# Performance work log

Hardware: AMD Instinct MI355X
Metric: run time of the kernel (lower is better)

Reference implementation:

```python
import jax, jax.numpy as jnp
import numpy as np


def setup_inputs() -> dict:
    key = jax.random.key(0)
    k1, k2 = jax.random.split(key)
    B, F = 131072, 32
    LOCAL_DIM, RANK, UNITS = 2, 10, 8
    X = jax.random.normal(k1, (B, F), dtype=jnp.float32)
    kernel = jax.random.normal(k2, (LOCAL_DIM, RANK, F, UNITS), dtype=jnp.float32) * 0.24  # ~glorot for fan sizes here
    return {"X": X, "kernel": kernel}


def reference(X, kernel):
    # X: [B, F]; kernel: [local_dim, rank, F, units]
    local_dim = kernel.shape[0]
    # powers X^0 .. X^(local_dim-1), stacked on last axis -> [B, F, local_dim]
    powers = jnp.stack([X ** p for p in range(local_dim)], axis=-1)
    # L2-normalize over the power axis (matches tf.sqrt(reduce_sum(x**2)))
    norms = jnp.sqrt(jnp.sum(powers * powers, axis=-1, keepdims=True))
    x = powers / norms  # [B, F, local_dim]
    # per-feature matmul across all units at once: [B, F, rank, units]
    t = jnp.einsum('bfd,drfu->bfru', x, kernel)
    # hadamard product over features, then sum over CP rank -> [B, units]
    out = jnp.sum(jnp.prod(t, axis=1), axis=1)
    return out  # activation is linear (None)
```

## Files before the change

kernel.cpp:

```cpp
#include <hip/hip_runtime.h>


typedef float f32x2 __attribute__((ext_vector_type(2)));
typedef float f32x4 __attribute__((ext_vector_type(4)));

#define F 32
#define RANK 10
#define UNITS 8
#define YSPLIT 5

__global__ __launch_bounds__(320) void cp_based_kernel(
    const float* __restrict__ X,
    const float* __restrict__ K,
    float* __restrict__ out,
    int B)
{
    __shared__ float red[YSPLIT][64][UNITS];

    const int lane = threadIdx.x;
    const int y = __builtin_amdgcn_readfirstlane(threadIdx.y);
    const int b = blockIdx.x * 64 + lane;

    const f32x4* xrow = reinterpret_cast<const f32x4*>(X + (size_t)b * F);
    float xv[F];
#pragma unroll
    for (int i = 0; i < F / 4; ++i) {
        f32x4 v = xrow[i];
#pragma unroll
        for (int j = 0; j < 4; ++j) xv[i * 4 + j] = v[j];
    }

    const int K1_OFF = RANK * F * UNITS;

    f32x2 s0 = {0.f, 0.f}, s1 = {0.f, 0.f}, s2 = {0.f, 0.f}, s3 = {0.f, 0.f};

#pragma unroll
    for (int rr = 0; rr < 2; ++rr) {
        const int r = 2 * y + rr;
        const float* k0b = K + r * F * UNITS;
        const float* k1b = k0b + K1_OFF;
        f32x2 p0 = {1.f, 1.f}, p1 = {1.f, 1.f}, p2 = {1.f, 1.f}, p3 = {1.f, 1.f};
#pragma unroll
        for (int f = 0; f < F; ++f) {
            const f32x2* k0 = reinterpret_cast<const f32x2*>(k0b + f * UNITS);
            const f32x2* k1 = reinterpret_cast<const f32x2*>(k1b + f * UNITS);
            float xf = xv[f];
            f32x2 xs = {xf, xf};
            f32x2 t0 = xs * k1[0] + k0[0];
            f32x2 t1 = xs * k1[1] + k0[1];
            f32x2 t2 = xs * k1[2] + k0[2];
            f32x2 t3 = xs * k1[3] + k0[3];
            p0 *= t0;
            p1 *= t1;
            p2 *= t2;
            p3 *= t3;
        }
        s0 += p0; s1 += p1; s2 += p2; s3 += p3;
    }

    f32x4* redp = reinterpret_cast<f32x4*>(&red[y][lane][0]);
    redp[0] = f32x4{s0[0], s0[1], s1[0], s1[1]};
    redp[1] = f32x4{s2[0], s2[1], s3[0], s3[1]};
    __syncthreads();

    if (y == 0) {
        f32x4 a0 = redp[0];
        f32x4 a1 = redp[1];
#pragma unroll
        for (int k = 1; k < YSPLIT; ++k) {
            const f32x4* q = reinterpret_cast<const f32x4*>(&red[k][lane][0]);
            a0 += q[0];
            a1 += q[1];
        }
        float pA = 1.0f, pB = 1.0f;
#pragma unroll
        for (int f = 0; f < 16; ++f) pA *= __builtin_fmaf(xv[f], xv[f], 1.0f);
#pragma unroll
        for (int f = 16; f < 32; ++f) pB *= __builtin_fmaf(xv[f], xv[f], 1.0f);
        float pn = __builtin_amdgcn_rsqf(pA) * __builtin_amdgcn_rsqf(pB);
        a0 *= pn;
        a1 *= pn;
        f32x4* o = reinterpret_cast<f32x4*>(out + (size_t)b * UNITS);
        o[0] = a0;
        o[1] = a1;
    }
}

extern "C" void kernel_launch(void* const* d_in, const int* in_sizes, int n_in,
                              void* d_out, int out_size, void* d_ws, size_t ws_size,
                              hipStream_t stream) {
    const float* X = (const float*)d_in[0];
    const float* K = (const float*)d_in[1];
    float* out = (float*)d_out;
    int B = in_sizes[0] / F;

    dim3 block(64, YSPLIT);
    dim3 grid(B / 64);
    hipLaunchKernelGGL(cp_based_kernel, grid, block, 0, stream, X, K, out, B);
}
```

Measured before the change: 31.20 us.

## Assign one wave per CP rank and process four row batches per thread

The block becomes 64x10 threads, one wave per rank instead of two ranks per wave, and each thread now handles four rows. X is streamed in float4 chunks rather than held as a full 32-float register row, and each kernel-weight vector load is reused across four rows. The norm product is folded into the same chunk loop on wave 0. The cost is a much larger LDS reduction buffer (about 80 KB per block), which limits blocks per CU, plus a longer serial reduction over ten ranks.

```diff
diff --git a/kernel.cpp b/kernel.cpp
--- a/kernel.cpp
+++ b/kernel.cpp
@@ -1,88 +1,95 @@
 #include <hip/hip_runtime.h>
 
 
-typedef float f32x2 __attribute__((ext_vector_type(2)));
 typedef float f32x4 __attribute__((ext_vector_type(4)));
 
 #define F 32
 #define RANK 10
 #define UNITS 8
-#define YSPLIT 5
+#define NB 4
+#define ROWS (64 * NB)
 
-__global__ __launch_bounds__(320) void cp_based_kernel(
+__global__ __launch_bounds__(64 * RANK) void cp_based_kernel(
     const float* __restrict__ X,
     const float* __restrict__ K,
     float* __restrict__ out,
     int B)
 {
-    __shared__ float red[YSPLIT][64][UNITS];
+    __shared__ f32x4 red[RANK][2][NB][64];
 
     const int lane = threadIdx.x;
     const int y = __builtin_amdgcn_readfirstlane(threadIdx.y);
-    const int b = blockIdx.x * 64 + lane;
+    const long rowbase = (long)blockIdx.x * ROWS;
 
-    const f32x4* xrow = reinterpret_cast<const f32x4*>(X + (size_t)b * F);
-    float xv[F];
+    const float* k0b = K + y * (F * UNITS);
+    const float* k1b = K + RANK * F * UNITS + y * (F * UNITS);
+
+    f32x4 p[NB][2];
+    float np[NB];
 #pragma unroll
-    for (int i = 0; i < F / 4; ++i) {
-        f32x4 v = xrow[i];
-#pragma unroll
-        for (int j = 0; j < 4; ++j) xv[i * 4 + j] = v[j];
+    for (int i = 0; i < NB; ++i) {
+        p[i][0] = f32x4{1.f, 1.f, 1.f, 1.f};
+        p[i][1] = f32x4{1.f, 1.f, 1.f, 1.f};
+        np[i] = 1.f;
     }
 
-    const int K1_OFF = RANK * F * UNITS;
+#pragma unroll
+    for (int jc = 0; jc < F / 4; ++jc) {
+        f32x4 xw[NB];
+#pragma unroll
+        for (int i = 0; i < NB; ++i)
+            xw[i] = *reinterpret_cast<const f32x4*>(
+                X + (rowbase + i * 64 + lane) * F + jc * 4);
 
-    f32x2 s0 = {0.f, 0.f}, s1 = {0.f, 0.f}, s2 = {0.f, 0.f}, s3 = {0.f, 0.f};
+        if (y == 0) {
+#pragma unroll
+            for (int i = 0; i < NB; ++i)
+#pragma unroll
+                for (int jf = 0; jf < 4; ++jf)
+                    np[i] *= __builtin_fmaf(xw[i][jf], xw[i][jf], 1.0f);
+        }
 
 #pragma unroll
-    for (int rr = 0; rr < 2; ++rr) {
-        const int r = 2 * y + rr;
-        const float* k0b = K + r * F * UNITS;
-        const float* k1b = k0b + K1_OFF;
-        f32x2 p0 = {1.f, 1.f}, p1 = {1.f, 1.f}, p2 = {1.f, 1.f}, p3 = {1.f, 1.f};
+        for (int jf = 0; jf < 4; ++jf) {
+            const int f = jc * 4 + jf;
+            f32x4 k0a = *reinterpret_cast<const f32x4*>(k0b + f * UNITS);
+            f32x4 k0c = *reinterpret_cast<const f32x4*>(k0b + f * UNITS + 4);
+            f32x4 k1a = *reinterpret_cast<const f32x4*>(k1b + f * UNITS);
+            f32x4 k1c = *reinterpret_cast<const f32x4*>(k1b + f * UNITS + 4);
 #pragma unroll
-        for (int f = 0; f < F; ++f) {
-            const f32x2* k0 = reinterpret_cast<const f32x2*>(k0b + f * UNITS);
-            const f32x2* k1 = reinterpret_cast<const f32x2*>(k1b + f * UNITS);
-            float xf = xv[f];
-            f32x2 xs = {xf, xf};
-            f32x2 t0 = xs * k1[0] + k0[0];
-            f32x2 t1 = xs * k1[1] + k0[1];
-            f32x2 t2 = xs * k1[2] + k0[2];
-            f32x2 t3 = xs * k1[3] + k0[3];
-            p0 *= t0;
-            p1 *= t1;
-            p2 *= t2;
-            p3 *= t3;
+            for (int i = 0; i < NB; ++i) {
+                float x = xw[i][jf];
+                f32x4 xs = {x, x, x, x};
+                p[i][0] *= xs * k1a + k0a;
+                p[i][1] *= xs * k1c + k0c;
+            }
         }
-        s0 += p0; s1 += p1; s2 += p2; s3 += p3;
     }
 
-    f32x4* redp = reinterpret_cast<f32x4*>(&red[y][lane][0]);
-    redp[0] = f32x4{s0[0], s0[1], s1[0], s1[1]};
-    redp[1] = f32x4{s2[0], s2[1], s3[0], s3[1]};
+#pragma unroll
+    for (int i = 0; i < NB; ++i) {
+        red[y][0][i][lane] = p[i][0];
+        red[y][1][i][lane] = p[i][1];
+    }
     __syncthreads();
 
     if (y == 0) {
-        f32x4 a0 = redp[0];
-        f32x4 a1 = redp[1];
 #pragma unroll
-        for (int k = 1; k < YSPLIT; ++k) {
-            const f32x4* q = reinterpret_cast<const f32x4*>(&red[k][lane][0]);
-            a0 += q[0];
-            a1 += q[1];
+        for (int i = 0; i < NB; ++i) {
+            f32x4 a0 = red[0][0][i][lane];
+            f32x4 a1 = red[0][1][i][lane];
+#pragma unroll
+            for (int k = 1; k < RANK; ++k) {
+                a0 += red[k][0][i][lane];
+                a1 += red[k][1][i][lane];
+            }
+            float pn = __builtin_amdgcn_rsqf(np[i]);
+            a0 *= pn;
+            a1 *= pn;
+            f32x4* o = reinterpret_cast<f32x4*>(out + (rowbase + i * 64 + lane) * UNITS);
+            o[0] = a0;
+            o[1] = a1;
         }
-        float pA = 1.0f, pB = 1.0f;
-#pragma unroll
-        for (int f = 0; f < 16; ++f) pA *= __builtin_fmaf(xv[f], xv[f], 1.0f);
-#pragma unroll
-        for (int f = 16; f < 32; ++f) pB *= __builtin_fmaf(xv[f], xv[f], 1.0f);
-        float pn = __builtin_amdgcn_rsqf(pA) * __builtin_amdgcn_rsqf(pB);
-        a0 *= pn;
-        a1 *= pn;
-        f32x4* o = reinterpret_cast<f32x4*>(out + (size_t)b * UNITS);
-        o[0] = a0;
-        o[1] = a1;
     }
 }
 
@@ -94,7 +101,7 @@
     float* out = (float*)d_out;
     int B = in_sizes[0] / F;
 
-    dim3 block(64, YSPLIT);
-    dim3 grid(B / 64);
+    dim3 block(64, RANK);
+    dim3 grid(B / ROWS);
     hipLaunchKernelGGL(cp_based_kernel, grid, block, 0, stream, X, K, out, B);
 }
```

Result: slower. 99.17 us (+217.9%).
